# Performance work log

Hardware: AMD Instinct MI355X
Metric: run time of the kernel (lower is better)

Reference implementation:

```python
import jax, jax.numpy as jnp
import numpy as np

D_MODEL = 1024
HEADS = 16
D_HEAD = D_MODEL // HEADS


def setup_inputs() -> dict:
    key = jax.random.key(0)
    ks = jax.random.split(key, 7)
    s = 1.0 / np.sqrt(D_MODEL)
    x = jax.random.normal(ks[0], (4, 2048, D_MODEL), dtype=jnp.float32)
    Wq = jax.random.uniform(ks[1], (D_MODEL, D_MODEL), jnp.float32, -s, s)
    bq = jax.random.uniform(ks[2], (D_MODEL,), jnp.float32, -s, s)
    Wk = jax.random.uniform(ks[3], (D_MODEL, D_MODEL), jnp.float32, -s, s)
    bk = jax.random.uniform(ks[4], (D_MODEL,), jnp.float32, -s, s)
    Wv = jax.random.uniform(ks[5], (D_MODEL, D_MODEL), jnp.float32, -s, s)
    bv = jax.random.uniform(ks[6], (D_MODEL,), jnp.float32, -s, s)
    return {"x": x, "Wq": Wq, "bq": bq, "Wk": Wk, "bk": bk, "Wv": Wv, "bv": bv}


def reference(x, Wq, bq, Wk, bk, Wv, bv):
    B, S, D = x.shape
    # QKV projections, split heads: [B, H, S, Dh]
    def split(t):
        return t.reshape(B, S, HEADS, D_HEAD).transpose(0, 2, 1, 3)
    q = split(x @ Wq + bq)
    k = split(x @ Wk + bk)
    v = split(x @ Wv + bv)
    scores = jnp.einsum('bhqd,bhkd->bhqk', q, k) / np.sqrt(D_HEAD).astype(jnp.float32)
    attn = jax.nn.softmax(scores, axis=-1)
    out = jnp.einsum('bhqk,bhkd->bhqd', attn, v)
    return out.transpose(0, 2, 1, 3).reshape(B, S, D)
```

## Files before the change

### kernel.cpp

```cpp
#include <hip/hip_runtime.h>

typedef _Float16 f16;
typedef __attribute__((ext_vector_type(2))) _Float16 f16x2;
typedef __attribute__((ext_vector_type(2))) __fp16   hf16x2;
typedef __attribute__((ext_vector_type(4))) _Float16 f16x4;
typedef __attribute__((ext_vector_type(8))) _Float16 f16x8;
typedef __attribute__((ext_vector_type(4))) float    f32x4;

#define D_MODEL 1024
#define HEADS   16
#define DH      64
#define SEQ     2048
#define BATCH   4
#define SSCALE  0.1803368801111204f

__device__ __forceinline__ void gload_lds16(const void* g, void* lds) {
  __builtin_amdgcn_global_load_lds(
      (const __attribute__((address_space(1))) unsigned int*)g,
      (__attribute__((address_space(3))) unsigned int*)lds, 16, 0, 0);
}

__global__ __launch_bounds__(256) void cast_x_kernel(const float* __restrict__ x,
                                                     f16* __restrict__ xb) {
  int i = blockIdx.x * 256 + threadIdx.x;
  float4 v = ((const float4*)x)[i];
  f16x4 h;
  h[0] = (f16)v.x; h[1] = (f16)v.y; h[2] = (f16)v.z; h[3] = (f16)v.w;
  ((f16x4*)xb)[i] = h;
}

__global__ __launch_bounds__(256) void wtrans_kernel(const float* __restrict__ Wq,
                                                     const float* __restrict__ Wk,
                                                     const float* __restrict__ Wv,
                                                     f16* __restrict__ wt) {
  const float* W = blockIdx.z == 0 ? Wq : (blockIdx.z == 1 ? Wk : Wv);
  f16* out = wt + (size_t)blockIdx.z * D_MODEL * D_MODEL;
  __shared__ float tile[64][65];
  int n0 = blockIdx.x * 64, k0 = blockIdx.y * 64;
  int tx = threadIdx.x & 63, ty = threadIdx.x >> 6;
#pragma unroll
  for (int r = 0; r < 16; ++r)
    tile[ty * 16 + r][tx] = W[(size_t)(k0 + ty * 16 + r) * D_MODEL + n0 + tx];
  __syncthreads();
#pragma unroll
  for (int r = 0; r < 16; ++r)
    out[(size_t)(n0 + ty * 16 + r) * D_MODEL + k0 + tx] = (f16)tile[tx][ty * 16 + r];
}

__global__ __launch_bounds__(512, 2) void qkv_gemm_kernel(
    const f16* __restrict__ xb, const f16* __restrict__ wt_all,
    const float* __restrict__ bq, const float* __restrict__ bk, const float* __restrict__ bv,
    f16* __restrict__ qout, f16* __restrict__ kout, f16* __restrict__ vtout) {
  const int z = blockIdx.z;
  const f16* wt = wt_all + (size_t)z * D_MODEL * D_MODEL;
  const float* bias = z == 0 ? bq : (z == 1 ? bk : bv);
  const int n0 = blockIdx.x * 256, m0 = blockIdx.y * 256;

  __shared__ f16 As[2][256 * 32];
  __shared__ f16 Bs[2][256 * 32];

  const int tid = threadIdx.x;
  const int lane = tid & 63, w = tid >> 6;
  const int quad = lane >> 4, l15 = lane & 15;
  const int wm = w & 1, wn = w >> 1;

  const int pce = (quad ^ (l15 & 3)) * 8;
  const int aoff = wm * 4096 + l15 * 32 + pce;
  const int boff = wn * 2048 + l15 * 32 + pce;

  int srow[2], scl[2];
#pragma unroll
  for (int c = 0; c < 2; ++c) {
    int slot = (w * 2 + c) * 64 + lane;
    srow[c] = slot >> 2;
    scl[c] = (slot & 3) ^ (srow[c] & 3);
  }

  f32x4 acc[8][4];
#pragma unroll
  for (int i = 0; i < 8; ++i)
#pragma unroll
    for (int j = 0; j < 4; ++j) acc[i][j] = (f32x4){0.f, 0.f, 0.f, 0.f};

#pragma unroll
  for (int c = 0; c < 2; ++c) {
    gload_lds16(xb + (size_t)(m0 + srow[c]) * D_MODEL + scl[c] * 8, &As[0][(w * 2 + c) * 512]);
    gload_lds16(wt + (size_t)(n0 + srow[c]) * D_MODEL + scl[c] * 8, &Bs[0][(w * 2 + c) * 512]);
  }

  for (int k0 = 0; k0 < D_MODEL; k0 += 32) {
    const int buf = (k0 >> 5) & 1;
    const int kn = (k0 + 32) & (D_MODEL - 1);
    __syncthreads();
#pragma unroll
    for (int c = 0; c < 2; ++c) {
      gload_lds16(xb + (size_t)(m0 + srow[c]) * D_MODEL + kn + scl[c] * 8, &As[buf ^ 1][(w * 2 + c) * 512]);
      gload_lds16(wt + (size_t)(n0 + srow[c]) * D_MODEL + kn + scl[c] * 8, &Bs[buf ^ 1][(w * 2 + c) * 512]);
    }
    f16x8 a[8], b[4];
#pragma unroll
    for (int mt = 0; mt < 8; ++mt) a[mt] = *(const f16x8*)(&As[buf][aoff + mt * 512]);
#pragma unroll
    for (int nt = 0; nt < 4; ++nt) b[nt] = *(const f16x8*)(&Bs[buf][boff + nt * 512]);
#pragma unroll
    for (int mt = 0; mt < 8; ++mt)
#pragma unroll
      for (int nt = 0; nt < 4; ++nt)
        acc[mt][nt] = __builtin_amdgcn_mfma_f32_16x16x32_f16(a[mt], b[nt], acc[mt][nt], 0, 0, 0);
  }

  const float sc = (z == 0) ? SSCALE : 1.0f;
  float bcol[4];
#pragma unroll
  for (int nt = 0; nt < 4; ++nt) bcol[nt] = bias[n0 + wn * 64 + nt * 16 + l15];

  if (z < 2) {
    f16* out = (z == 0) ? qout : kout;
#pragma unroll
    for (int mt = 0; mt < 8; ++mt) {
      int mbase = m0 + wm * 128 + mt * 16 + quad * 4;
#pragma unroll
      for (int nt = 0; nt < 4; ++nt) {
        int n = n0 + wn * 64 + nt * 16 + l15;
        int h = n >> 6, dh = n & 63;
#pragma unroll
        for (int r = 0; r < 4; ++r) {
          int m = mbase + r;
          int b = m >> 11, s = m & 2047;
          out[((size_t)(b * HEADS + h) * SEQ + s) * DH + dh] = (f16)((acc[mt][nt][r] + bcol[nt]) * sc);
        }
      }
    }
  } else {
#pragma unroll
    for (int mt = 0; mt < 8; ++mt) {
      int mbase = m0 + wm * 128 + mt * 16 + quad * 4;
      int b = mbase >> 11, s = mbase & 2047;
#pragma unroll
      for (int nt = 0; nt < 4; ++nt) {
        int n = n0 + wn * 64 + nt * 16 + l15;
        int h = n >> 6, dh = n & 63;
        f16x4 v;
#pragma unroll
        for (int r = 0; r < 4; ++r) v[r] = (f16)(acc[mt][nt][r] + bcol[nt]);
        *(f16x4*)(vtout + ((size_t)(b * HEADS + h) * DH + dh) * SEQ + s) = v;
      }
    }
  }
}

__global__ __launch_bounds__(256, 4) void attn_kernel(
    const f16* __restrict__ q, const f16* __restrict__ k, const f16* __restrict__ vt,
    float* __restrict__ out) {
  const int bh = blockIdx.x;
  const int s0 = blockIdx.y * 128;
  const int b = bh >> 4, h = bh & 15;
  const int tid = threadIdx.x, lane = tid & 63, w = tid >> 6;
  const int quad = lane >> 4, l15 = lane & 15;
  const int qh = quad >> 1, q1 = quad & 1;

  __shared__ f16 Ks[2][64 * 64];
  __shared__ f16 Vs[2][64 * 64];

  const f16* qbase = q + ((size_t)bh * SEQ + s0 + w * 32) * DH;
  const f16* kbase = k + (size_t)bh * SEQ * DH;
  const f16* vbase = vt + (size_t)bh * DH * SEQ;

  f16x8 qf[2][2];
#pragma unroll
  for (int qt = 0; qt < 2; ++qt)
#pragma unroll
    for (int ks = 0; ks < 2; ++ks)
      qf[qt][ks] = *(const f16x8*)(qbase + (qt * 16 + l15) * DH + ks * 32 + quad * 8);

  int koff[2];
  koff[0] = l15 * 64 + ((quad ^ (l15 & 7)) * 8);
  koff[1] = l15 * 64 + (((4 + quad) ^ (l15 & 7)) * 8);
  int voff[4];
#pragma unroll
  for (int ks = 0; ks < 4; ++ks)
    voff[ks] = l15 * 64 + (((ks * 2 + qh) ^ (l15 & 7)) * 8) + q1 * 4;

  int srow[2], scl[2];
#pragma unroll
  for (int c = 0; c < 2; ++c) {
    int slot = (w * 2 + c) * 64 + lane;
    srow[c] = slot >> 3;
    scl[c] = (slot & 7) ^ (srow[c] & 7);
  }

  float lsum[2] = {0.f, 0.f};
  f32x4 o[4][2];
#pragma unroll
  for (int i = 0; i < 4; ++i)
#pragma unroll
    for (int j = 0; j < 2; ++j) o[i][j] = (f32x4){0.f, 0.f, 0.f, 0.f};

#pragma unroll
  for (int c = 0; c < 2; ++c) {
    gload_lds16(kbase + (size_t)srow[c] * DH + scl[c] * 8, &Ks[0][(w * 2 + c) * 512]);
    gload_lds16(vbase + (size_t)srow[c] * SEQ + scl[c] * 8, &Vs[0][(w * 2 + c) * 512]);
  }

  for (int kt = 0; kt < SEQ / 64; ++kt) {
    const int buf = kt & 1;
    const int ktn = (kt + 1) & (SEQ / 64 - 1);
    __syncthreads();
#pragma unroll
    for (int c = 0; c < 2; ++c) {
      gload_lds16(kbase + (size_t)(ktn * 64 + srow[c]) * DH + scl[c] * 8, &Ks[buf ^ 1][(w * 2 + c) * 512]);
      gload_lds16(vbase + (size_t)srow[c] * SEQ + ktn * 64 + scl[c] * 8, &Vs[buf ^ 1][(w * 2 + c) * 512]);
    }

    f32x4 st[4][2];
#pragma unroll
    for (int mt = 0; mt < 4; ++mt)
#pragma unroll
      for (int qt = 0; qt < 2; ++qt) st[mt][qt] = (f32x4){0.f, 0.f, 0.f, 0.f};
#pragma unroll
    for (int mt = 0; mt < 4; ++mt)
#pragma unroll
      for (int ks = 0; ks < 2; ++ks) {
        f16x8 af = *(const f16x8*)(&Ks[buf][koff[ks] + mt * 1024]);
#pragma unroll
        for (int qt = 0; qt < 2; ++qt)
          st[mt][qt] = __builtin_amdgcn_mfma_f32_16x16x32_f16(af, qf[qt][ks], st[mt][qt], 0, 0, 0);
      }

#pragma unroll
    for (int ks = 0; ks < 4; ++ks) {
      f16x4 pb[2];
#pragma unroll
      for (int qt = 0; qt < 2; ++qt) {
        float e0 = __builtin_amdgcn_exp2f(st[ks][qt][0]);
        float e1 = __builtin_amdgcn_exp2f(st[ks][qt][1]);
        float e2 = __builtin_amdgcn_exp2f(st[ks][qt][2]);
        float e3 = __builtin_amdgcn_exp2f(st[ks][qt][3]);
        lsum[qt] += (e0 + e1) + (e2 + e3);
        hf16x2 h01 = __builtin_amdgcn_cvt_pkrtz(e0, e1);
        hf16x2 h23 = __builtin_amdgcn_cvt_pkrtz(e2, e3);
        f16x2 p01 = __builtin_bit_cast(f16x2, h01);
        f16x2 p23 = __builtin_bit_cast(f16x2, h23);
        pb[qt][0] = p01[0]; pb[qt][1] = p01[1]; pb[qt][2] = p23[0]; pb[qt][3] = p23[1];
      }
#pragma unroll
      for (int mt = 0; mt < 4; ++mt) {
        f16x4 va = *(const f16x4*)(&Vs[buf][voff[ks] + mt * 1024]);
#pragma unroll
        for (int qt = 0; qt < 2; ++qt)
          o[mt][qt] = __builtin_amdgcn_mfma_f32_16x16x16f16(va, pb[qt], o[mt][qt], 0, 0, 0);
      }
    }
  }

#pragma unroll
  for (int qt = 0; qt < 2; ++qt) {
    float l = lsum[qt];
    l += __shfl_xor(l, 16, 64);
    l += __shfl_xor(l, 32, 64);
    float inv = 1.f / l;
    int sq = s0 + w * 32 + qt * 16 + l15;
    float* obase = out + ((size_t)b * SEQ + sq) * D_MODEL + h * DH;
#pragma unroll
    for (int mt = 0; mt < 4; ++mt) {
      f32x4 vv;
#pragma unroll
      for (int r = 0; r < 4; ++r) vv[r] = o[mt][qt][r] * inv;
      *(f32x4*)(obase + mt * 16 + quad * 4) = vv;
    }
  }
}

extern "C" void kernel_launch(void* const* d_in, const int* in_sizes, int n_in,
                              void* d_out, int out_size, void* d_ws, size_t ws_size,
                              hipStream_t stream) {
  const float* x  = (const float*)d_in[0];
  const float* Wq = (const float*)d_in[1];
  const float* bq = (const float*)d_in[2];
  const float* Wk = (const float*)d_in[3];
  const float* bk = (const float*)d_in[4];
  const float* Wv = (const float*)d_in[5];
  const float* bv = (const float*)d_in[6];
  float* out = (float*)d_out;

  char* ws = (char*)d_ws;
  f16* xb = (f16*)ws;
  f16* wt = (f16*)(ws + (size_t)16 * 1024 * 1024);
  f16* q  = (f16*)(ws + (size_t)22 * 1024 * 1024);
  f16* kk = q + (size_t)BATCH * SEQ * D_MODEL;
  f16* vt = kk + (size_t)BATCH * SEQ * D_MODEL;

  cast_x_kernel<<<8192, 256, 0, stream>>>(x, xb);
  wtrans_kernel<<<dim3(16, 16, 3), 256, 0, stream>>>(Wq, Wk, Wv, wt);
  qkv_gemm_kernel<<<dim3(4, 32, 3), 512, 0, stream>>>(xb, wt, bq, bk, bv, q, kk, vt);
  attn_kernel<<<dim3(64, 16), 256, 0, stream>>>(q, kk, vt, out);
}
```

Measured before the change: 289.3 us.

## Merge prep kernels, shrink QKV GEMM tiles to 128x128, tidy P packing

Folds the x cast and weight transpose into a single launch to save one kernel launch. The QKV GEMM moves from 256x256 tiles with 512 threads to 128x128 tiles with 256 threads, with a new LDS swizzle. This gives 1536 blocks instead of 384, for better load balance and occupancy across CUs, at the cost of lower operand reuse per tile. It also rewrites how the packed fp16 probabilities are assembled in the attention kernel.

```diff
diff --git a/kernel.cpp b/kernel.cpp
--- a/kernel.cpp
+++ b/kernel.cpp
@@ -20,23 +20,26 @@
       (__attribute__((address_space(3))) unsigned int*)lds, 16, 0, 0);
 }
 
-__global__ __launch_bounds__(256) void cast_x_kernel(const float* __restrict__ x,
-                                                     f16* __restrict__ xb) {
-  int i = blockIdx.x * 256 + threadIdx.x;
-  float4 v = ((const float4*)x)[i];
-  f16x4 h;
-  h[0] = (f16)v.x; h[1] = (f16)v.y; h[2] = (f16)v.z; h[3] = (f16)v.w;
-  ((f16x4*)xb)[i] = h;
-}
-
-__global__ __launch_bounds__(256) void wtrans_kernel(const float* __restrict__ Wq,
-                                                     const float* __restrict__ Wk,
-                                                     const float* __restrict__ Wv,
-                                                     f16* __restrict__ wt) {
-  const float* W = blockIdx.z == 0 ? Wq : (blockIdx.z == 1 ? Wk : Wv);
-  f16* out = wt + (size_t)blockIdx.z * D_MODEL * D_MODEL;
+__global__ __launch_bounds__(256) void prep_kernel(const float* __restrict__ x,
+                                                   const float* __restrict__ Wq,
+                                                   const float* __restrict__ Wk,
+                                                   const float* __restrict__ Wv,
+                                                   f16* __restrict__ xb,
+                                                   f16* __restrict__ wt) {
+  if (blockIdx.x < 8192) {
+    int i = blockIdx.x * 256 + threadIdx.x;
+    float4 v = ((const float4*)x)[i];
+    f16x4 h;
+    h[0] = (f16)v.x; h[1] = (f16)v.y; h[2] = (f16)v.z; h[3] = (f16)v.w;
+    ((f16x4*)xb)[i] = h;
+    return;
+  }
+  int bid = blockIdx.x - 8192;
+  int z = bid >> 8, rem = bid & 255;
+  const float* W = z == 0 ? Wq : (z == 1 ? Wk : Wv);
+  f16* out = wt + (size_t)z * D_MODEL * D_MODEL;
   __shared__ float tile[64][65];
-  int n0 = blockIdx.x * 64, k0 = blockIdx.y * 64;
+  int n0 = (rem & 15) * 64, k0 = (rem >> 4) * 64;
   int tx = threadIdx.x & 63, ty = threadIdx.x >> 6;
 #pragma unroll
   for (int r = 0; r < 16; ++r)
@@ -47,25 +50,25 @@
     out[(size_t)(n0 + ty * 16 + r) * D_MODEL + k0 + tx] = (f16)tile[tx][ty * 16 + r];
 }
 
-__global__ __launch_bounds__(512, 2) void qkv_gemm_kernel(
+__global__ __launch_bounds__(256, 3) void qkv_gemm_kernel(
     const f16* __restrict__ xb, const f16* __restrict__ wt_all,
     const float* __restrict__ bq, const float* __restrict__ bk, const float* __restrict__ bv,
     f16* __restrict__ qout, f16* __restrict__ kout, f16* __restrict__ vtout) {
   const int z = blockIdx.z;
   const f16* wt = wt_all + (size_t)z * D_MODEL * D_MODEL;
   const float* bias = z == 0 ? bq : (z == 1 ? bk : bv);
-  const int n0 = blockIdx.x * 256, m0 = blockIdx.y * 256;
-
-  __shared__ f16 As[2][256 * 32];
-  __shared__ f16 Bs[2][256 * 32];
+  const int n0 = blockIdx.x * 128, m0 = blockIdx.y * 128;
+
+  __shared__ f16 As[2][128 * 32];
+  __shared__ f16 Bs[2][128 * 32];
 
   const int tid = threadIdx.x;
   const int lane = tid & 63, w = tid >> 6;
   const int quad = lane >> 4, l15 = lane & 15;
   const int wm = w & 1, wn = w >> 1;
 
-  const int pce = (quad ^ (l15 & 3)) * 8;
-  const int aoff = wm * 4096 + l15 * 32 + pce;
+  const int pce = (quad ^ ((l15 >> 1) & 3)) * 8;
+  const int aoff = wm * 2048 + l15 * 32 + pce;
   const int boff = wn * 2048 + l15 * 32 + pce;
 
   int srow[2], scl[2];
@@ -73,12 +76,12 @@
   for (int c = 0; c < 2; ++c) {
     int slot = (w * 2 + c) * 64 + lane;
     srow[c] = slot >> 2;
-    scl[c] = (slot & 3) ^ (srow[c] & 3);
-  }
-
-  f32x4 acc[8][4];
-#pragma unroll
-  for (int i = 0; i < 8; ++i)
+    scl[c] = (slot & 3) ^ ((srow[c] >> 1) & 3);
+  }
+
+  f32x4 acc[4][4];
+#pragma unroll
+  for (int i = 0; i < 4; ++i)
 #pragma unroll
     for (int j = 0; j < 4; ++j) acc[i][j] = (f32x4){0.f, 0.f, 0.f, 0.f};
 
@@ -97,13 +100,13 @@
       gload_lds16(xb + (size_t)(m0 + srow[c]) * D_MODEL + kn + scl[c] * 8, &As[buf ^ 1][(w * 2 + c) * 512]);
       gload_lds16(wt + (size_t)(n0 + srow[c]) * D_MODEL + kn + scl[c] * 8, &Bs[buf ^ 1][(w * 2 + c) * 512]);
     }
-    f16x8 a[8], b[4];
-#pragma unroll
-    for (int mt = 0; mt < 8; ++mt) a[mt] = *(const f16x8*)(&As[buf][aoff + mt * 512]);
+    f16x8 a[4], b[4];
+#pragma unroll
+    for (int mt = 0; mt < 4; ++mt) a[mt] = *(const f16x8*)(&As[buf][aoff + mt * 512]);
 #pragma unroll
     for (int nt = 0; nt < 4; ++nt) b[nt] = *(const f16x8*)(&Bs[buf][boff + nt * 512]);
 #pragma unroll
-    for (int mt = 0; mt < 8; ++mt)
+    for (int mt = 0; mt < 4; ++mt)
 #pragma unroll
       for (int nt = 0; nt < 4; ++nt)
         acc[mt][nt] = __builtin_amdgcn_mfma_f32_16x16x32_f16(a[mt], b[nt], acc[mt][nt], 0, 0, 0);
@@ -117,8 +120,8 @@
   if (z < 2) {
     f16* out = (z == 0) ? qout : kout;
 #pragma unroll
-    for (int mt = 0; mt < 8; ++mt) {
-      int mbase = m0 + wm * 128 + mt * 16 + quad * 4;
+    for (int mt = 0; mt < 4; ++mt) {
+      int mbase = m0 + wm * 64 + mt * 16 + quad * 4;
 #pragma unroll
       for (int nt = 0; nt < 4; ++nt) {
         int n = n0 + wn * 64 + nt * 16 + l15;
@@ -133,8 +136,8 @@
     }
   } else {
 #pragma unroll
-    for (int mt = 0; mt < 8; ++mt) {
-      int mbase = m0 + wm * 128 + mt * 16 + quad * 4;
+    for (int mt = 0; mt < 4; ++mt) {
+      int mbase = m0 + wm * 64 + mt * 16 + quad * 4;
       int b = mbase >> 11, s = mbase & 2047;
 #pragma unroll
       for (int nt = 0; nt < 4; ++nt) {
@@ -237,11 +240,9 @@
         float e2 = __builtin_amdgcn_exp2f(st[ks][qt][2]);
         float e3 = __builtin_amdgcn_exp2f(st[ks][qt][3]);
         lsum[qt] += (e0 + e1) + (e2 + e3);
-        hf16x2 h01 = __builtin_amdgcn_cvt_pkrtz(e0, e1);
-        hf16x2 h23 = __builtin_amdgcn_cvt_pkrtz(e2, e3);
-        f16x2 p01 = __builtin_bit_cast(f16x2, h01);
-        f16x2 p23 = __builtin_bit_cast(f16x2, h23);
-        pb[qt][0] = p01[0]; pb[qt][1] = p01[1]; pb[qt][2] = p23[0]; pb[qt][3] = p23[1];
+        f16x2 p01 = __builtin_bit_cast(f16x2, __builtin_amdgcn_cvt_pkrtz(e0, e1));
+        f16x2 p23 = __builtin_bit_cast(f16x2, __builtin_amdgcn_cvt_pkrtz(e2, e3));
+        pb[qt] = __builtin_shufflevector(p01, p23, 0, 1, 2, 3);
       }
 #pragma unroll
       for (int mt = 0; mt < 4; ++mt) {
@@ -290,8 +291,7 @@
   f16* kk = q + (size_t)BATCH * SEQ * D_MODEL;
   f16* vt = kk + (size_t)BATCH * SEQ * D_MODEL;
 
-  cast_x_kernel<<<8192, 256, 0, stream>>>(x, xb);
-  wtrans_kernel<<<dim3(16, 16, 3), 256, 0, stream>>>(Wq, Wk, Wv, wt);
-  qkv_gemm_kernel<<<dim3(4, 32, 3), 512, 0, stream>>>(xb, wt, bq, bk, bv, q, kk, vt);
+  prep_kernel<<<8192 + 768, 256, 0, stream>>>(x, Wq, Wk, Wv, xb, wt);
+  qkv_gemm_kernel<<<dim3(8, 64, 3), 256, 0, stream>>>(xb, wt, bq, bk, bv, q, kk, vt);
   attn_kernel<<<dim3(64, 16), 256, 0, stream>>>(q, kk, vt, out);
 }
```

Result: faster. 265.3 us (-8.3%).
